# Kernel optimization log

Hardware: AMD Instinct MI355X
Metric: run time of the kernel (lower is better)

## Reference

```python
import jax, jax.numpy as jnp
import numpy as np

B, N, C, E, K = 2, 1024, 128, 64, 20

def setup_inputs() -> dict:
    key = jax.random.key(0)
    ks = jax.random.split(key, 4)
    x = jax.random.normal(ks[0], (B, N, C), dtype=jnp.float32)
    Wl = jax.random.normal(ks[1], (C, E), dtype=jnp.float32) * 0.05
    Wr = jax.random.normal(ks[2], (C, E), dtype=jnp.float32) * 0.05
    att = jax.random.normal(ks[3], (1, E), dtype=jnp.float32) * 0.1
    bl = jnp.zeros((E,), dtype=jnp.float32)
    br = jnp.zeros((E,), dtype=jnp.float32)
    edge_index = jnp.zeros((2, 1), dtype=jnp.int64)
    batch = jnp.zeros((B * N,), dtype=jnp.int64)
    return {"x": x, "Wl": Wl, "bl": bl, "Wr": Wr, "br": br, "att": att,
            "edge_index": edge_index, "batch": batch}

def reference(x, Wl, bl, Wr, br, att, edge_index, batch):
    # x: [B, N, C]
    b, n, _ = x.shape
    x_l = x @ Wl + bl              # [B, N, E]
    x_r = x @ Wr + br              # [B, N, E]
    # dense pairwise scores: leaky_relu(x_l_i + x_r_j) . att  -> [B, N, N]
    x_cat = jax.nn.leaky_relu(x_l[:, :, None, :] + x_r[:, None, :, :], 0.2)
    alpha = jnp.einsum('bijd,d->bij', x_cat, att[0])
    alpha = jnp.nan_to_num(alpha, nan=0.0, posinf=0.0, neginf=0.0)
    k = min(K, n)
    vals, idx = jax.lax.top_k(alpha, k)            # [B, N, k]
    attention = jax.nn.softmax(vals, axis=-1).reshape(-1)  # [B*N*k]
    # edge index construction (dropout p used only in training; eval = identity)
    offset = (jnp.arange(b) * n)[:, None]                      # [B, 1]
    index_i = jnp.tile(jnp.repeat(jnp.arange(n), k)[None, :], (b, 1)) + offset
    index_j = idx.reshape(b, n * k) + offset
    new_edge_index = jnp.stack([index_i.reshape(-1), index_j.reshape(-1)], axis=0)
    return new_edge_index, attention
```

## Files before the change

### kernel.cpp

```cpp
#include <hip/hip_runtime.h>

#define Bq 2
#define Nq 1024
#define Cq 128
#define Eq 64
#define Kq 20
#define TI 8
#define BNK (Bq * Nq * Kq)
#define NEGF (-3.0e38f)

#define DPP_F(x, ctrl) __int_as_float(__builtin_amdgcn_update_dpp( \
    __float_as_int(x), __float_as_int(x), (ctrl), 0xf, 0xf, false))
#define DPP_I(x, ctrl) __builtin_amdgcn_update_dpp((x), (x), (ctrl), 0xf, 0xf, false)
#define RL_F(x, l) __int_as_float(__builtin_amdgcn_readlane(__float_as_int(x), (l)))
#define RL_I(x, l) __builtin_amdgcn_readlane((x), (l))
#define QP_XOR1 0xB1
#define QP_XOR2 0x4E
#define ROR4    0x124
#define ROR8    0x128

__global__ __launch_bounds__(128) void proj_kernel(
    const float* __restrict__ x, const float* __restrict__ Wl,
    const float* __restrict__ bl, const float* __restrict__ Wr,
    const float* __restrict__ br, const float* __restrict__ att,
    float* __restrict__ xl, float* __restrict__ xrT, float* __restrict__ rdot) {
  const int r0 = blockIdx.x * 4;
  const int t = threadIdx.x;
  const int e = t & 63;
  const bool left = (t < 64);
  const float* __restrict__ W = left ? Wl : Wr;
  const float* __restrict__ xrow = x + (size_t)r0 * Cq;

  float acc[4] = {0.f, 0.f, 0.f, 0.f};
#pragma unroll 8
  for (int c4 = 0; c4 < Cq / 4; ++c4) {
    const float4 xa = *(const float4*)&xrow[c4 * 4];
    const float4 xb = *(const float4*)&xrow[Cq + c4 * 4];
    const float4 xc = *(const float4*)&xrow[2 * Cq + c4 * 4];
    const float4 xd = *(const float4*)&xrow[3 * Cq + c4 * 4];
    const float a0[4] = {xa.x, xa.y, xa.z, xa.w};
    const float a1[4] = {xb.x, xb.y, xb.z, xb.w};
    const float a2[4] = {xc.x, xc.y, xc.z, xc.w};
    const float a3[4] = {xd.x, xd.y, xd.z, xd.w};
#pragma unroll
    for (int dd = 0; dd < 4; ++dd) {
      const float w = W[(c4 * 4 + dd) * Eq + e];
      acc[0] = fmaf(a0[dd], w, acc[0]);
      acc[1] = fmaf(a1[dd], w, acc[1]);
      acc[2] = fmaf(a2[dd], w, acc[2]);
      acc[3] = fmaf(a3[dd], w, acc[3]);
    }
  }
  const float bias = left ? bl[e] : br[e];
#pragma unroll
  for (int k = 0; k < 4; ++k) acc[k] += bias;

  if (left) {
#pragma unroll
    for (int k = 0; k < 4; ++k) xl[(size_t)(r0 + k) * Eq + e] = acc[k];
  } else {
    const float ae = att[e];
#pragma unroll
    for (int k = 0; k < 4; ++k) {
      xrT[(size_t)e * (Bq * Nq) + r0 + k] = acc[k];
      float s = acc[k] * ae;
      s += DPP_F(s, QP_XOR1);
      s += DPP_F(s, QP_XOR2);
      s += DPP_F(s, ROR4);
      s += DPP_F(s, ROR8);
      const float sd = (RL_F(s, 0) + RL_F(s, 16)) + (RL_F(s, 32) + RL_F(s, 48));
      if (e == 0) rdot[r0 + k] = sd;
    }
  }
}

__global__ __launch_bounds__(512) void attn_kernel(
    const float* __restrict__ xl, const float* __restrict__ xrT,
    const float* __restrict__ rdot, const float* __restrict__ att,
    float* __restrict__ out) {
  const int gi0  = blockIdx.x * TI;
  const int b    = gi0 >> 10;
  const int tid  = threadIdx.x;
  const int lane = tid & 63;
  const int wave = tid >> 6;

  __shared__ float alpha[TI][Nq];
  __shared__ float xls[TI][Eq];

  xls[tid >> 6][tid & 63] = xl[(size_t)gi0 * Eq + tid];
  __syncthreads();

  {
    const int jt = tid & 255;
    const int j0 = jt * 4;
    const int rg = tid >> 8;
    const float4 rd4 = *(const float4*)&rdot[b * Nq + j0];
    const float rdv[4] = {rd4.x, rd4.y, rd4.z, rd4.w};
    float acc[4][4];
#pragma unroll
    for (int rr = 0; rr < 4; ++rr)
#pragma unroll
      for (int jj = 0; jj < 4; ++jj) acc[rr][jj] = 1.5f * rdv[jj];

    const float* __restrict__ xrb = xrT + (size_t)b * Nq + j0;
    for (int ch = 0; ch < 16; ++ch) {
      const float4 av4 = *(const float4*)&att[ch * 4];
      const float av[4] = {av4.x, av4.y, av4.z, av4.w};
      float xlr[4][4];
#pragma unroll
      for (int rr = 0; rr < 4; ++rr) {
        const float4 v = *(const float4*)&xls[rg * 4 + rr][ch * 4];
        xlr[rr][0] = v.x; xlr[rr][1] = v.y; xlr[rr][2] = v.z; xlr[rr][3] = v.w;
      }
#pragma unroll
      for (int dd = 0; dd < 4; ++dd) {
        const float4 xv4 = *(const float4*)&xrb[(size_t)(ch * 4 + dd) * (Bq * Nq)];
        const float xv[4] = {xv4.x, xv4.y, xv4.z, xv4.w};
        const float a = av[dd];
#pragma unroll
        for (int rr = 0; rr < 4; ++rr) {
          const float xld = xlr[rr][dd];
#pragma unroll
          for (int jj = 0; jj < 4; ++jj)
            acc[rr][jj] = fmaf(fabsf(xld + xv[jj]), a, acc[rr][jj]);
        }
      }
    }
#pragma unroll
    for (int rr = 0; rr < 4; ++rr)
      *(float4*)&alpha[rg * 4 + rr][j0] =
          make_float4(acc[rr][0], acc[rr][1], acc[rr][2], acc[rr][3]);
  }
  __syncthreads();

  float vals[16];
#pragma unroll
  for (int s = 0; s < 16; ++s) vals[s] = alpha[wave][lane + 64 * s];

  float lv = vals[0];
  int   pk = lane;
#pragma unroll
  for (int s = 1; s < 16; ++s)
    if (vals[s] > lv) { lv = vals[s]; pk = (s << 6) | lane; }

  float m0 = 0.f, ssum = 0.f, myv = 0.f;
  int myi = 0;
#pragma unroll 1
  for (int round = 0; round < Kq; ++round) {
    float m = lv;
    m = fmaxf(m, DPP_F(m, QP_XOR1));
    m = fmaxf(m, DPP_F(m, QP_XOR2));
    m = fmaxf(m, DPP_F(m, ROR4));
    m = fmaxf(m, DPP_F(m, ROR8));
    const float bv = fmaxf(fmaxf(RL_F(m, 0), RL_F(m, 16)),
                           fmaxf(RL_F(m, 32), RL_F(m, 48)));
    int key = (lv == bv) ? pk : 0x7FFFFFFF;
    key = min(key, DPP_I(key, QP_XOR1));
    key = min(key, DPP_I(key, QP_XOR2));
    key = min(key, DPP_I(key, ROR4));
    key = min(key, DPP_I(key, ROR8));
    const int jsel = min(min(RL_I(key, 0), RL_I(key, 16)),
                         min(RL_I(key, 32), RL_I(key, 48)));
    if (round == 0) m0 = bv;
    ssum += __expf(0.4f * (bv - m0));
    if (lane == round) { myv = bv; myi = jsel; }
    if (lane == (jsel & 63)) {
      const int sk = jsel >> 6;
#pragma unroll
      for (int s = 0; s < 16; ++s)
        if (s == sk) vals[s] = NEGF;
      lv = vals[0]; pk = lane;
#pragma unroll
      for (int s = 1; s < 16; ++s)
        if (vals[s] > lv) { lv = vals[s]; pk = (s << 6) | lane; }
    }
  }

  if (lane < Kq) {
    const int gi = gi0 + wave;
    const float p = __expf(0.4f * (myv - m0)) / ssum;
    const int base = gi * Kq + lane;
    out[base]            = (float)gi;
    out[BNK + base]      = (float)(b * Nq + myi);
    out[2 * BNK + base]  = p;
  }
}

extern "C" void kernel_launch(void* const* d_in, const int* in_sizes, int n_in,
                              void* d_out, int out_size, void* d_ws, size_t ws_size,
                              hipStream_t stream) {
  const float* x   = (const float*)d_in[0];
  const float* Wl  = (const float*)d_in[1];
  const float* bl  = (const float*)d_in[2];
  const float* Wr  = (const float*)d_in[3];
  const float* br  = (const float*)d_in[4];
  const float* att = (const float*)d_in[5];
  float* out = (float*)d_out;

  float* xl   = (float*)d_ws;
  float* xrT  = xl + (size_t)Bq * Nq * Eq;
  float* rdot = xrT + (size_t)Eq * Bq * Nq;

  proj_kernel<<<(Bq * Nq) / 4, 128, 0, stream>>>(x, Wl, bl, Wr, br, att, xl, xrT, rdot);
  attn_kernel<<<(Bq * Nq) / TI, 512, 0, stream>>>(xl, xrT, rdot, att, out);
}
```

Baseline: 41.29 us.

## Use one row per projection block and double attn threads per block

The projection kernel now handles one row per block, staging that row in shared memory, instead of four rows per block. This gives four times more blocks but reloads the weights for every row. The attention kernel now runs 1024 threads per block, with each thread scoring 2 rows instead of 4, which lowers per-thread register pressure and raises parallelism in the scoring phase. The top-k phase still uses only 8 waves, so the other half of the block sits idle there.

```diff
diff --git a/kernel.cpp b/kernel.cpp
--- a/kernel.cpp
+++ b/kernel.cpp
@@ -24,57 +24,33 @@
     const float* __restrict__ bl, const float* __restrict__ Wr,
     const float* __restrict__ br, const float* __restrict__ att,
     float* __restrict__ xl, float* __restrict__ xrT, float* __restrict__ rdot) {
-  const int r0 = blockIdx.x * 4;
+  const int row = blockIdx.x;
   const int t = threadIdx.x;
   const int e = t & 63;
   const bool left = (t < 64);
+  __shared__ float xs[Cq];
+  xs[t] = x[(size_t)row * Cq + t];
+  __syncthreads();
   const float* __restrict__ W = left ? Wl : Wr;
-  const float* __restrict__ xrow = x + (size_t)r0 * Cq;
-
-  float acc[4] = {0.f, 0.f, 0.f, 0.f};
+  float acc = 0.f;
 #pragma unroll 8
-  for (int c4 = 0; c4 < Cq / 4; ++c4) {
-    const float4 xa = *(const float4*)&xrow[c4 * 4];
-    const float4 xb = *(const float4*)&xrow[Cq + c4 * 4];
-    const float4 xc = *(const float4*)&xrow[2 * Cq + c4 * 4];
-    const float4 xd = *(const float4*)&xrow[3 * Cq + c4 * 4];
-    const float a0[4] = {xa.x, xa.y, xa.z, xa.w};
-    const float a1[4] = {xb.x, xb.y, xb.z, xb.w};
-    const float a2[4] = {xc.x, xc.y, xc.z, xc.w};
-    const float a3[4] = {xd.x, xd.y, xd.z, xd.w};
-#pragma unroll
-    for (int dd = 0; dd < 4; ++dd) {
-      const float w = W[(c4 * 4 + dd) * Eq + e];
-      acc[0] = fmaf(a0[dd], w, acc[0]);
-      acc[1] = fmaf(a1[dd], w, acc[1]);
-      acc[2] = fmaf(a2[dd], w, acc[2]);
-      acc[3] = fmaf(a3[dd], w, acc[3]);
-    }
-  }
-  const float bias = left ? bl[e] : br[e];
-#pragma unroll
-  for (int k = 0; k < 4; ++k) acc[k] += bias;
-
+  for (int c = 0; c < Cq; ++c) acc = fmaf(xs[c], W[c * Eq + e], acc);
+  acc += left ? bl[e] : br[e];
   if (left) {
-#pragma unroll
-    for (int k = 0; k < 4; ++k) xl[(size_t)(r0 + k) * Eq + e] = acc[k];
+    xl[(size_t)row * Eq + e] = acc;
   } else {
-    const float ae = att[e];
-#pragma unroll
-    for (int k = 0; k < 4; ++k) {
-      xrT[(size_t)e * (Bq * Nq) + r0 + k] = acc[k];
-      float s = acc[k] * ae;
-      s += DPP_F(s, QP_XOR1);
-      s += DPP_F(s, QP_XOR2);
-      s += DPP_F(s, ROR4);
-      s += DPP_F(s, ROR8);
-      const float sd = (RL_F(s, 0) + RL_F(s, 16)) + (RL_F(s, 32) + RL_F(s, 48));
-      if (e == 0) rdot[r0 + k] = sd;
-    }
+    xrT[(size_t)e * (Bq * Nq) + row] = acc;
+    float s = acc * att[e];
+    s += DPP_F(s, QP_XOR1);
+    s += DPP_F(s, QP_XOR2);
+    s += DPP_F(s, ROR4);
+    s += DPP_F(s, ROR8);
+    const float sd = (RL_F(s, 0) + RL_F(s, 16)) + (RL_F(s, 32) + RL_F(s, 48));
+    if (e == 0) rdot[row] = sd;
   }
 }
 
-__global__ __launch_bounds__(512) void attn_kernel(
+__global__ __launch_bounds__(1024) void attn_kernel(
     const float* __restrict__ xl, const float* __restrict__ xrT,
     const float* __restrict__ rdot, const float* __restrict__ att,
     float* __restrict__ out) {
@@ -87,102 +63,97 @@
   __shared__ float alpha[TI][Nq];
   __shared__ float xls[TI][Eq];
 
-  xls[tid >> 6][tid & 63] = xl[(size_t)gi0 * Eq + tid];
+  if (tid < TI * Eq) xls[tid >> 6][tid & 63] = xl[(size_t)gi0 * Eq + tid];
   __syncthreads();
 
   {
     const int jt = tid & 255;
     const int j0 = jt * 4;
-    const int rg = tid >> 8;
+    const int r0 = (tid >> 8) * 2;
     const float4 rd4 = *(const float4*)&rdot[b * Nq + j0];
-    const float rdv[4] = {rd4.x, rd4.y, rd4.z, rd4.w};
-    float acc[4][4];
-#pragma unroll
-    for (int rr = 0; rr < 4; ++rr)
-#pragma unroll
-      for (int jj = 0; jj < 4; ++jj) acc[rr][jj] = 1.5f * rdv[jj];
+    float acc0[4], acc1[4];
+    acc0[0] = 1.5f * rd4.x; acc0[1] = 1.5f * rd4.y;
+    acc0[2] = 1.5f * rd4.z; acc0[3] = 1.5f * rd4.w;
+    acc1[0] = acc0[0]; acc1[1] = acc0[1]; acc1[2] = acc0[2]; acc1[3] = acc0[3];
 
     const float* __restrict__ xrb = xrT + (size_t)b * Nq + j0;
+#pragma unroll
     for (int ch = 0; ch < 16; ++ch) {
       const float4 av4 = *(const float4*)&att[ch * 4];
-      const float av[4] = {av4.x, av4.y, av4.z, av4.w};
-      float xlr[4][4];
-#pragma unroll
-      for (int rr = 0; rr < 4; ++rr) {
-        const float4 v = *(const float4*)&xls[rg * 4 + rr][ch * 4];
-        xlr[rr][0] = v.x; xlr[rr][1] = v.y; xlr[rr][2] = v.z; xlr[rr][3] = v.w;
-      }
+      const float4 xla = *(const float4*)&xls[r0][ch * 4];
+      const float4 xlb = *(const float4*)&xls[r0 + 1][ch * 4];
+      const float av[4]  = {av4.x, av4.y, av4.z, av4.w};
+      const float la[4]  = {xla.x, xla.y, xla.z, xla.w};
+      const float lb[4]  = {xlb.x, xlb.y, xlb.z, xlb.w};
 #pragma unroll
       for (int dd = 0; dd < 4; ++dd) {
         const float4 xv4 = *(const float4*)&xrb[(size_t)(ch * 4 + dd) * (Bq * Nq)];
         const float xv[4] = {xv4.x, xv4.y, xv4.z, xv4.w};
         const float a = av[dd];
 #pragma unroll
-        for (int rr = 0; rr < 4; ++rr) {
-          const float xld = xlr[rr][dd];
-#pragma unroll
-          for (int jj = 0; jj < 4; ++jj)
-            acc[rr][jj] = fmaf(fabsf(xld + xv[jj]), a, acc[rr][jj]);
+        for (int jj = 0; jj < 4; ++jj) {
+          acc0[jj] = fmaf(fabsf(la[dd] + xv[jj]), a, acc0[jj]);
+          acc1[jj] = fmaf(fabsf(lb[dd] + xv[jj]), a, acc1[jj]);
         }
       }
     }
-#pragma unroll
-    for (int rr = 0; rr < 4; ++rr)
-      *(float4*)&alpha[rg * 4 + rr][j0] =
-          make_float4(acc[rr][0], acc[rr][1], acc[rr][2], acc[rr][3]);
+    *(float4*)&alpha[r0][j0]     = make_float4(acc0[0], acc0[1], acc0[2], acc0[3]);
+    *(float4*)&alpha[r0 + 1][j0] = make_float4(acc1[0], acc1[1], acc1[2], acc1[3]);
   }
   __syncthreads();
 
-  float vals[16];
+  if (wave < TI) {
+    float vals[16];
 #pragma unroll
-  for (int s = 0; s < 16; ++s) vals[s] = alpha[wave][lane + 64 * s];
+    for (int s = 0; s < 16; ++s) vals[s] = alpha[wave][lane + 64 * s];
 
-  float lv = vals[0];
-  int   pk = lane;
+    float lv = vals[0];
+    int   pk = lane;
 #pragma unroll
-  for (int s = 1; s < 16; ++s)
-    if (vals[s] > lv) { lv = vals[s]; pk = (s << 6) | lane; }
+    for (int s = 1; s < 16; ++s)
+      if (vals[s] > lv) { lv = vals[s]; pk = (s << 6) | lane; }
 
-  float m0 = 0.f, ssum = 0.f, myv = 0.f;
-  int myi = 0;
+    float m0 = 0.f, ssum = 0.f, myv = 0.f;
+    int myi = 0;
 #pragma unroll 1
-  for (int round = 0; round < Kq; ++round) {
-    float m = lv;
-    m = fmaxf(m, DPP_F(m, QP_XOR1));
-    m = fmaxf(m, DPP_F(m, QP_XOR2));
-    m = fmaxf(m, DPP_F(m, ROR4));
-    m = fmaxf(m, DPP_F(m, ROR8));
-    const float bv = fmaxf(fmaxf(RL_F(m, 0), RL_F(m, 16)),
-                           fmaxf(RL_F(m, 32), RL_F(m, 48)));
-    int key = (lv == bv) ? pk : 0x7FFFFFFF;
-    key = min(key, DPP_I(key, QP_XOR1));
-    key = min(key, DPP_I(key, QP_XOR2));
-    key = min(key, DPP_I(key, ROR4));
-    key = min(key, DPP_I(key, ROR8));
-    const int jsel = min(min(RL_I(key, 0), RL_I(key, 16)),
-                         min(RL_I(key, 32), RL_I(key, 48)));
-    if (round == 0) m0 = bv;
-    ssum += __expf(0.4f * (bv - m0));
-    if (lane == round) { myv = bv; myi = jsel; }
-    if (lane == (jsel & 63)) {
-      const int sk = jsel >> 6;
+    for (int round = 0; round < Kq; ++round) {
+      float m = lv;
+      m = fmaxf(m, DPP_F(m, QP_XOR1));
+      m = fmaxf(m, DPP_F(m, QP_XOR2));
+      m = fmaxf(m, DPP_F(m, ROR4));
+      m = fmaxf(m, DPP_F(m, ROR8));
+      const float bv = fmaxf(fmaxf(RL_F(m, 0), RL_F(m, 16)),
+                             fmaxf(RL_F(m, 32), RL_F(m, 48)));
+      int key = (lv == bv) ? pk : 0x7FFFFFFF;
+      key = min(key, DPP_I(key, QP_XOR1));
+      key = min(key, DPP_I(key, QP_XOR2));
+      key = min(key, DPP_I(key, ROR4));
+      key = min(key, DPP_I(key, ROR8));
+      const int jsel = min(min(RL_I(key, 0), RL_I(key, 16)),
+                           min(RL_I(key, 32), RL_I(key, 48)));
+      if (round == 0) m0 = bv;
+      ssum += __expf(0.4f * (bv - m0));
+      if (lane == round) { myv = bv; myi = jsel; }
+      if (lane == (jsel & 63)) {
+        const int sk = jsel >> 6;
 #pragma unroll
-      for (int s = 0; s < 16; ++s)
-        if (s == sk) vals[s] = NEGF;
-      lv = vals[0]; pk = lane;
+        for (int s = 0; s < 16; ++s)
+          if (s == sk) vals[s] = NEGF;
+        lv = vals[0]; pk = lane;
 #pragma unroll
-      for (int s = 1; s < 16; ++s)
-        if (vals[s] > lv) { lv = vals[s]; pk = (s << 6) | lane; }
+        for (int s = 1; s < 16; ++s)
+          if (vals[s] > lv) { lv = vals[s]; pk = (s << 6) | lane; }
+      }
     }
-  }
 
-  if (lane < Kq) {
-    const int gi = gi0 + wave;
-    const float p = __expf(0.4f * (myv - m0)) / ssum;
-    const int base = gi * Kq + lane;
-    out[base]            = (float)gi;
-    out[BNK + base]      = (float)(b * Nq + myi);
-    out[2 * BNK + base]  = p;
+    if (lane < Kq) {
+      const int gi = gi0 + wave;
+      const float p = __expf(0.4f * (myv - m0)) / ssum;
+      const int base = gi * Kq + lane;
+      out[base]            = (float)gi;
+      out[BNK + base]      = (float)(b * Nq + myi);
+      out[2 * BNK + base]  = p;
+    }
   }
 }
 
@@ -201,6 +172,6 @@
   float* xrT  = xl + (size_t)Bq * Nq * Eq;
   float* rdot = xrT + (size_t)Eq * Bq * Nq;
 
-  proj_kernel<<<(Bq * Nq) / 4, 128, 0, stream>>>(x, Wl, bl, Wr, br, att, xl, xrT, rdot);
-  attn_kernel<<<(Bq * Nq) / TI, 512, 0, stream>>>(xl, xrT, rdot, att, out);
+  proj_kernel<<<Bq * Nq, 128, 0, stream>>>(x, Wl, bl, Wr, br, att, xl, xrT, rdot);
+  attn_kernel<<<(Bq * Nq) / TI, 1024, 0, stream>>>(xl, xrT, rdot, att, out);
 }
```

New measurement: 41.91 us. Within noise of the previous version (+1.5%).
